# Optimization experiments

Measured on AMD Instinct MI355X. Metric: run time of the kernel, lower is better.

Reference implementation:

```python
import jax, jax.numpy as jnp
import numpy as np

B, T = 4, 96
IN_DIM, OUT_DIM, HID = 16, 16, 16
REL = 2 * IN_DIM  # until=True -> cat(interval max, interval min)
BIG = 1e9


def interval_pooling(a, reduction):
    # a: [b, t, t, d]; out[b,i,j] = reduce over a[b,k,l] for all i<=k<=l<=j
    t = a.shape[1]
    mask = jnp.triu(jnp.ones((t, t), dtype=bool))[None, :, :, None]
    if reduction == 'max':
        fill, cum = -BIG, jax.lax.cummax
    else:
        fill, cum = BIG, jax.lax.cummin
    x = jnp.where(mask, a, fill)
    x = cum(x, axis=1, reverse=True)  # over start k >= i
    x = cum(x, axis=2)                # over end   l <= j
    return jnp.where(mask, x, 0.0)


def dp_step(f, r, W, b):
    # linear_input[b,i,k,j] = cat(f[b,i,k], r[b,k,j]); MLPLogic = Linear+sigmoid;
    # transition_pooling_2d1d = max over k (dim 2). Split W so the wide cubic
    # concat is never materialized (same math as cat + matmul).
    df = f.shape[-1]
    Wf, Wr = W[:df], W[df:]
    ft = jnp.einsum('bikd,dh->bikh', f, Wf)[:, :, :, None, :]  # [b,i,k,1,h]
    rt = jnp.einsum('bkjd,dh->bkjh', r, Wr)[:, None, :, :, :]  # [b,1,k,j,h]
    g = jax.nn.sigmoid(ft + rt + b)  # [b, t+1, t+1, t+1, h] cubic intermediate
    return jnp.max(g, axis=2)        # pool over transition point k


def setup_inputs() -> dict:
    key = jax.random.key(0)
    ks = jax.random.split(key, 7)
    a = jax.random.normal(ks[0], (B, T, T, IN_DIM), jnp.float32)
    W0 = 0.1 * jax.random.normal(ks[1], (REL + REL, HID), jnp.float32)
    b0 = 0.1 * jax.random.normal(ks[2], (HID,), jnp.float32)
    W1 = 0.1 * jax.random.normal(ks[3], (HID + REL + REL, HID), jnp.float32)
    b1 = 0.1 * jax.random.normal(ks[4], (HID,), jnp.float32)
    W2 = 0.1 * jax.random.normal(ks[5], (HID + REL, OUT_DIM), jnp.float32)
    b2 = 0.1 * jax.random.normal(ks[6], (OUT_DIM,), jnp.float32)
    return {'a': a, 'W0': W0, 'b0': b0, 'W1': W1, 'b1': b1, 'W2': W2, 'b2': b2}


def reference(a, W0, b0, W1, b1, W2, b2):
    bsz, t = a.shape[0], a.shape[1]
    r = jnp.concatenate([interval_pooling(a, 'max'),
                         interval_pooling(a, 'min')], axis=-1)  # [b,t,t,2*in]
    f = jnp.zeros((bsz, t + 1, t + 1, r.shape[-1]), a.dtype)
    f = f.at[:, :-1, 1:].set(r)  # pad to boundary indexing [b,t+1,t+1,rel]
    r = f
    # step 0
    f = dp_step(f, r, W0, b0)
    f = jnp.concatenate([f, r], axis=-1)  # residual_input
    # step 1
    f = dp_step(f, r, W1, b1)
    f = jnp.concatenate([f, r], axis=-1)
    # final MLPLogic
    f = jax.nn.sigmoid(f @ W2 + b2)
    return f[:, :-1, 1:]
```

## Files before the change

kernel.cpp:

```cpp
#include <hip/hip_runtime.h>
#include <hip/hip_bf16.h>

#define RS   100
#define PLS  9700
#define NP   9409
#define LSTR 34

#define OFF_R   0
#define OFF_A   (OFF_R  + 4*32*PLS)
#define OFF_Bm  (OFF_A  + 4*16*PLS)
#define OFF_F1  (OFF_Bm + 4*16*PLS)
#define OFF_F2  (OFF_F1 + 4*16*PLS)

__device__ __forceinline__ float sigm(float x) { return 1.0f / (1.0f + __expf(-x)); }

__global__ __launch_bounds__(256) void pool_kernel(const float* __restrict__ a, float* __restrict__ R) {
    __shared__ float s[96][97];
    const int tid = threadIdx.x;
    const int b  = blockIdx.x >> 5;
    const int ch = blockIdx.x & 31;
    const int d  = ch & 15;
    const bool isMin = (ch >= 16);

    for (int idx = tid; idx < 96 * 96; idx += 256) {
        int i = idx / 96, j = idx - i * 96;
        float v = a[((size_t)(b * 96 + i) * 96 + j) * 16 + d];
        if (isMin) v = -v;
        s[i][j] = (j >= i) ? v : -1e30f;
    }
    __syncthreads();
    if (tid < 96) {
        int j = tid; float run = -1e30f;
#pragma unroll 4
        for (int i = 95; i >= 0; --i) { run = fmaxf(run, s[i][j]); s[i][j] = run; }
    }
    __syncthreads();
    if (tid < 96) {
        int i = tid; float run = -1e30f;
#pragma unroll 4
        for (int j = 0; j < 96; ++j) { run = fmaxf(run, s[i][j]); s[i][j] = run; }
    }
    __syncthreads();
    float* Rp = R + (size_t)blockIdx.x * PLS;
    for (int idx = tid; idx < 97 * 97; idx += 256) {
        int x = idx / 97, y = idx - x * 97;
        float v = 0.f;
        if (x <= 95 && y >= 1 && x <= y - 1) { v = s[x][y - 1]; if (isMin) v = -v; }
        Rp[x * RS + y] = v;
    }
}

__global__ __launch_bounds__(256) void proj0_kernel(const float* __restrict__ R, const float* __restrict__ W,
                                                    float* __restrict__ A, float* __restrict__ B) {
    const int by = blockIdx.y, b = by >> 3, hp = by & 7;
    const int h0 = hp * 2, h1 = h0 + 1;
    const int p = blockIdx.x * 256 + threadIdx.x;
    if (p >= NP) return;
    const int x = p / 97, y = p - x * 97;
    const int off = x * RS + y;
    const float* Rb = R + (size_t)b * 32 * PLS + off;
    float accA0 = 0.f, accA1 = 0.f, accB0 = 0.f, accB1 = 0.f;
#pragma unroll
    for (int d = 0; d < 32; ++d) {
        float rv = Rb[(size_t)d * PLS];
        accA0 += rv * W[d * 16 + h0];
        accA1 += rv * W[d * 16 + h1];
        accB0 += rv * W[(32 + d) * 16 + h0];
        accB1 += rv * W[(32 + d) * 16 + h1];
    }
    A[(size_t)(b * 16 + h0) * PLS + off] = accA0;
    A[(size_t)(b * 16 + h1) * PLS + off] = accA1;
    B[(size_t)(b * 16 + h0) * PLS + off] = accB0;
    B[(size_t)(b * 16 + h1) * PLS + off] = accB1;
}

__global__ __launch_bounds__(256) void proj1_kernel(const float* __restrict__ R, const float* __restrict__ F1,
                                                    const float* __restrict__ W,
                                                    float* __restrict__ A, float* __restrict__ B) {
    const int by = blockIdx.y, b = by >> 3, hp = by & 7;
    const int h0 = hp * 2, h1 = h0 + 1;
    const int p = blockIdx.x * 256 + threadIdx.x;
    if (p >= NP) return;
    const int x = p / 97, y = p - x * 97;
    const int off = x * RS + y;
    const float* Rb = R  + (size_t)b * 32 * PLS + off;
    const float* Fb = F1 + (size_t)b * 16 * PLS + off;
    float accA0 = 0.f, accA1 = 0.f, accB0 = 0.f, accB1 = 0.f;
#pragma unroll
    for (int c = 0; c < 16; ++c) {
        float fv = Fb[(size_t)c * PLS];
        accA0 += fv * W[c * 16 + h0];
        accA1 += fv * W[c * 16 + h1];
    }
#pragma unroll
    for (int d = 0; d < 32; ++d) {
        float rv = Rb[(size_t)d * PLS];
        accA0 += rv * W[(16 + d) * 16 + h0];
        accA1 += rv * W[(16 + d) * 16 + h1];
        accB0 += rv * W[(48 + d) * 16 + h0];
        accB1 += rv * W[(48 + d) * 16 + h1];
    }
    A[(size_t)(b * 16 + h0) * PLS + off] = accA0;
    A[(size_t)(b * 16 + h1) * PLS + off] = accA1;
    B[(size_t)(b * 16 + h0) * PLS + off] = accB0;
    B[(size_t)(b * 16 + h1) * PLS + off] = accB1;
}

__global__ __launch_bounds__(256) void maxplus_kernel(const float* __restrict__ A, const float* __restrict__ Bm,
                                                      const float* __restrict__ bias, float* __restrict__ F) {
    __shared__ alignas(16) float As[97 * LSTR];
    __shared__ alignas(16) float Bs[97 * LSTR];
    const int tid = threadIdx.x;
    const int bh = blockIdx.y;
    const int h  = bh & 15;
    const int i0 = (blockIdx.x & 3) * 32;
    const int j0 = (blockIdx.x >> 2) * 32;
    const float* Ab = A  + (size_t)bh * PLS;
    const float* Bb = Bm + (size_t)bh * PLS;

    for (int idx = tid; idx < 32 * 97; idx += 256) {
        int r = idx / 97, k = idx - r * 97;
        int ii = i0 + r;
        As[k * LSTR + r] = (ii < 97) ? Ab[ii * RS + k] : -1e30f;
    }
    for (int idx = tid; idx < 97 * 32; idx += 256) {
        int k = idx >> 5, c = idx & 31;
        int jj = j0 + c;
        Bs[k * LSTR + c] = (jj < 97) ? Bb[k * RS + jj] : -1e30f;
    }
    __syncthreads();

    const int ty = tid >> 4, tx = tid & 15;
    float a00 = -1e30f, a01 = -1e30f, a10 = -1e30f, a11 = -1e30f;

#pragma unroll 4
    for (int k = 0; k < 97; ++k) {
        const float2 a2 = *reinterpret_cast<const float2*>(&As[k * LSTR + ty * 2]);
        const float2 b2 = *reinterpret_cast<const float2*>(&Bs[k * LSTR + tx * 2]);
        a00 = fmaxf(a00, a2.x + b2.x);
        a01 = fmaxf(a01, a2.x + b2.y);
        a10 = fmaxf(a10, a2.y + b2.x);
        a11 = fmaxf(a11, a2.y + b2.y);
    }

    const float bb = bias[h];
    float* Fb = F + (size_t)bh * PLS;
    const int col0 = j0 + tx * 2;
    const int row0 = i0 + ty * 2;
    float v[2][2] = {{a00, a01}, {a10, a11}};
#pragma unroll
    for (int r = 0; r < 2; ++r) {
        const int row = row0 + r;
        if (row > 96) continue;
        if (col0 + 1 <= 96) {
            float2 o;
            o.x = sigm(v[r][0] + bb);
            o.y = sigm(v[r][1] + bb);
            *reinterpret_cast<float2*>(&Fb[row * RS + col0]) = o;
        } else if (col0 <= 96) {
            Fb[row * RS + col0] = sigm(v[r][0] + bb);
        }
    }
}

__global__ __launch_bounds__(256) void final_kernel(const float* __restrict__ R, const float* __restrict__ F2,
                                                    const float* __restrict__ W, const float* __restrict__ bias,
                                                    float* __restrict__ out) {
    const int p = blockIdx.x * 256 + threadIdx.x;
    if (p >= 4 * 96 * 96) return;
    const int oj = p % 96;
    const int t1 = p / 96;
    const int i  = t1 % 96;
    const int b  = t1 / 96;
    const int off = i * RS + (oj + 1);
    const float* Fb = F2 + (size_t)b * 16 * PLS + off;
    const float* Rb = R  + (size_t)b * 32 * PLS + off;
    float acc[16];
#pragma unroll
    for (int o = 0; o < 16; ++o) acc[o] = bias[o];
#pragma unroll
    for (int c = 0; c < 16; ++c) {
        const float fv = Fb[(size_t)c * PLS];
#pragma unroll
        for (int o = 0; o < 16; ++o) acc[o] += fv * W[c * 16 + o];
    }
#pragma unroll
    for (int d = 0; d < 32; ++d) {
        const float rv = Rb[(size_t)d * PLS];
#pragma unroll
        for (int o = 0; o < 16; ++o) acc[o] += rv * W[(16 + d) * 16 + o];
    }
    float4* dst = reinterpret_cast<float4*>(out + (size_t)p * 16);
#pragma unroll
    for (int q = 0; q < 4; ++q) {
        float4 v;
        v.x = sigm(acc[q * 4 + 0]);
        v.y = sigm(acc[q * 4 + 1]);
        v.z = sigm(acc[q * 4 + 2]);
        v.w = sigm(acc[q * 4 + 3]);
        dst[q] = v;
    }
}

extern "C" void kernel_launch(void* const* d_in, const int* in_sizes, int n_in,
                              void* d_out, int out_size, void* d_ws, size_t ws_size,
                              hipStream_t stream) {
    const float* a  = (const float*)d_in[0];
    const float* W0 = (const float*)d_in[1];
    const float* b0 = (const float*)d_in[2];
    const float* W1 = (const float*)d_in[3];
    const float* b1 = (const float*)d_in[4];
    const float* W2 = (const float*)d_in[5];
    const float* b2 = (const float*)d_in[6];
    float* ws = (float*)d_ws;
    float* out = (float*)d_out;

    hipLaunchKernelGGL(pool_kernel, dim3(128), dim3(256), 0, stream, a, ws + OFF_R);
    hipLaunchKernelGGL(proj0_kernel, dim3(37, 32), dim3(256), 0, stream,
                       ws + OFF_R, W0, ws + OFF_A, ws + OFF_Bm);
    hipLaunchKernelGGL(maxplus_kernel, dim3(16, 64), dim3(256), 0, stream,
                       ws + OFF_A, ws + OFF_Bm, b0, ws + OFF_F1);
    hipLaunchKernelGGL(proj1_kernel, dim3(37, 32), dim3(256), 0, stream,
                       ws + OFF_R, ws + OFF_F1, W1, ws + OFF_A, ws + OFF_Bm);
    hipLaunchKernelGGL(maxplus_kernel, dim3(16, 64), dim3(256), 0, stream,
                       ws + OFF_A, ws + OFF_Bm, b1, ws + OFF_F2);
    hipLaunchKernelGGL(final_kernel, dim3(144), dim3(256), 0, stream,
                       ws + OFF_R, ws + OFF_F2, W2, b2, out);
}
```

Measured before the change: 151.1 us.

## Precompute step-1 R projections early, widen maxplus tiles, split final kernel outputs

The R-dependent parts of both DP steps' projections are computed together in one kernel, so the second projection only adds the F1 contribution and re-reads far less of R. The max-plus kernel now gives each thread a 2x4 output tile with float4 B loads, which halves the block count and raises arithmetic per shared load. The final kernel spreads each output position over four threads, each producing four channels, to increase parallelism. In exchange the workspace holds two extra buffers and there is an extra read of the precomputed partial sums.

Measured after the change: 152.4 us. No clear change (+0.8%).

```diff
diff --git a/kernel.cpp b/kernel.cpp
--- a/kernel.cpp
+++ b/kernel.cpp
@@ -1,16 +1,18 @@
 #include <hip/hip_runtime.h>
-#include <hip/hip_bf16.h>
 
 #define RS   100
 #define PLS  9700
 #define NP   9409
-#define LSTR 34
+#define ASTR 34
+#define BSTR 68
 
 #define OFF_R   0
-#define OFF_A   (OFF_R  + 4*32*PLS)
-#define OFF_Bm  (OFF_A  + 4*16*PLS)
-#define OFF_F1  (OFF_Bm + 4*16*PLS)
-#define OFF_F2  (OFF_F1 + 4*16*PLS)
+#define OFF_A   (OFF_R   + 4*32*PLS)
+#define OFF_Bm  (OFF_A   + 4*16*PLS)
+#define OFF_F1  (OFF_Bm  + 4*16*PLS)
+#define OFF_F2  (OFF_F1  + 4*16*PLS)
+#define OFF_A1r (OFF_F2  + 4*16*PLS)
+#define OFF_B1  (OFF_A1r + 4*16*PLS)
 
 __device__ __forceinline__ float sigm(float x) { return 1.0f / (1.0f + __expf(-x)); }
 
@@ -50,8 +52,10 @@
     }
 }
 
-__global__ __launch_bounds__(256) void proj0_kernel(const float* __restrict__ R, const float* __restrict__ W,
-                                                    float* __restrict__ A, float* __restrict__ B) {
+__global__ __launch_bounds__(256) void projA_kernel(const float* __restrict__ R,
+                                                    const float* __restrict__ W0, const float* __restrict__ W1,
+                                                    float* __restrict__ A0, float* __restrict__ B0,
+                                                    float* __restrict__ A1r, float* __restrict__ B1) {
     const int by = blockIdx.y, b = by >> 3, hp = by & 7;
     const int h0 = hp * 2, h1 = h0 + 1;
     const int p = blockIdx.x * 256 + threadIdx.x;
@@ -59,106 +63,125 @@
     const int x = p / 97, y = p - x * 97;
     const int off = x * RS + y;
     const float* Rb = R + (size_t)b * 32 * PLS + off;
-    float accA0 = 0.f, accA1 = 0.f, accB0 = 0.f, accB1 = 0.f;
+    float aA00 = 0.f, aA01 = 0.f, aB00 = 0.f, aB01 = 0.f;
+    float aA10 = 0.f, aA11 = 0.f, aB10 = 0.f, aB11 = 0.f;
 #pragma unroll
     for (int d = 0; d < 32; ++d) {
-        float rv = Rb[(size_t)d * PLS];
-        accA0 += rv * W[d * 16 + h0];
-        accA1 += rv * W[d * 16 + h1];
-        accB0 += rv * W[(32 + d) * 16 + h0];
-        accB1 += rv * W[(32 + d) * 16 + h1];
-    }
-    A[(size_t)(b * 16 + h0) * PLS + off] = accA0;
-    A[(size_t)(b * 16 + h1) * PLS + off] = accA1;
-    B[(size_t)(b * 16 + h0) * PLS + off] = accB0;
-    B[(size_t)(b * 16 + h1) * PLS + off] = accB1;
-}
-
-__global__ __launch_bounds__(256) void proj1_kernel(const float* __restrict__ R, const float* __restrict__ F1,
-                                                    const float* __restrict__ W,
-                                                    float* __restrict__ A, float* __restrict__ B) {
+        const float rv = Rb[(size_t)d * PLS];
+        aA00 += rv * W0[d * 16 + h0];
+        aA01 += rv * W0[d * 16 + h1];
+        aB00 += rv * W0[(32 + d) * 16 + h0];
+        aB01 += rv * W0[(32 + d) * 16 + h1];
+        aA10 += rv * W1[(16 + d) * 16 + h0];
+        aA11 += rv * W1[(16 + d) * 16 + h1];
+        aB10 += rv * W1[(48 + d) * 16 + h0];
+        aB11 += rv * W1[(48 + d) * 16 + h1];
+    }
+    const size_t o0 = (size_t)(b * 16 + h0) * PLS + off;
+    const size_t o1 = (size_t)(b * 16 + h1) * PLS + off;
+    A0 [o0] = aA00;  A0 [o1] = aA01;
+    B0 [o0] = aB00;  B0 [o1] = aB01;
+    A1r[o0] = aA10;  A1r[o1] = aA11;
+    B1 [o0] = aB10;  B1 [o1] = aB11;
+}
+
+__global__ __launch_bounds__(256) void projF_kernel(const float* __restrict__ F1, const float* __restrict__ A1r,
+                                                    const float* __restrict__ W1, float* __restrict__ A) {
     const int by = blockIdx.y, b = by >> 3, hp = by & 7;
     const int h0 = hp * 2, h1 = h0 + 1;
     const int p = blockIdx.x * 256 + threadIdx.x;
     if (p >= NP) return;
     const int x = p / 97, y = p - x * 97;
     const int off = x * RS + y;
-    const float* Rb = R  + (size_t)b * 32 * PLS + off;
     const float* Fb = F1 + (size_t)b * 16 * PLS + off;
-    float accA0 = 0.f, accA1 = 0.f, accB0 = 0.f, accB1 = 0.f;
+    const size_t o0 = (size_t)(b * 16 + h0) * PLS + off;
+    const size_t o1 = (size_t)(b * 16 + h1) * PLS + off;
+    float a0 = A1r[o0], a1 = A1r[o1];
 #pragma unroll
     for (int c = 0; c < 16; ++c) {
-        float fv = Fb[(size_t)c * PLS];
-        accA0 += fv * W[c * 16 + h0];
-        accA1 += fv * W[c * 16 + h1];
-    }
-#pragma unroll
-    for (int d = 0; d < 32; ++d) {
-        float rv = Rb[(size_t)d * PLS];
-        accA0 += rv * W[(16 + d) * 16 + h0];
-        accA1 += rv * W[(16 + d) * 16 + h1];
-        accB0 += rv * W[(48 + d) * 16 + h0];
-        accB1 += rv * W[(48 + d) * 16 + h1];
-    }
-    A[(size_t)(b * 16 + h0) * PLS + off] = accA0;
-    A[(size_t)(b * 16 + h1) * PLS + off] = accA1;
-    B[(size_t)(b * 16 + h0) * PLS + off] = accB0;
-    B[(size_t)(b * 16 + h1) * PLS + off] = accB1;
+        const float fv = Fb[(size_t)c * PLS];
+        a0 += fv * W1[c * 16 + h0];
+        a1 += fv * W1[c * 16 + h1];
+    }
+    A[o0] = a0;
+    A[o1] = a1;
 }
 
 __global__ __launch_bounds__(256) void maxplus_kernel(const float* __restrict__ A, const float* __restrict__ Bm,
                                                       const float* __restrict__ bias, float* __restrict__ F) {
-    __shared__ alignas(16) float As[97 * LSTR];
-    __shared__ alignas(16) float Bs[97 * LSTR];
+    __shared__ alignas(16) float As[97 * ASTR];
+    __shared__ alignas(16) float Bs[97 * BSTR];
     const int tid = threadIdx.x;
     const int bh = blockIdx.y;
     const int h  = bh & 15;
     const int i0 = (blockIdx.x & 3) * 32;
-    const int j0 = (blockIdx.x >> 2) * 32;
+    const int j0 = (blockIdx.x >> 2) * 64;
     const float* Ab = A  + (size_t)bh * PLS;
     const float* Bb = Bm + (size_t)bh * PLS;
 
     for (int idx = tid; idx < 32 * 97; idx += 256) {
         int r = idx / 97, k = idx - r * 97;
         int ii = i0 + r;
-        As[k * LSTR + r] = (ii < 97) ? Ab[ii * RS + k] : -1e30f;
-    }
-    for (int idx = tid; idx < 97 * 32; idx += 256) {
-        int k = idx >> 5, c = idx & 31;
-        int jj = j0 + c;
-        Bs[k * LSTR + c] = (jj < 97) ? Bb[k * RS + jj] : -1e30f;
+        As[k * ASTR + r] = (ii <= 96) ? Ab[ii * RS + k] : -1e30f;
+    }
+    for (int idx = tid; idx < 97 * 16; idx += 256) {
+        int k = idx >> 4, q = idx & 15;
+        int jj = j0 + q * 4;
+        float4 v;
+        if (jj + 3 <= 96) {
+            v = *reinterpret_cast<const float4*>(&Bb[k * RS + jj]);
+        } else {
+            v.x = (jj     <= 96) ? Bb[k * RS + jj]     : -1e30f;
+            v.y = (jj + 1 <= 96) ? Bb[k * RS + jj + 1] : -1e30f;
+            v.z = (jj + 2 <= 96) ? Bb[k * RS + jj + 2] : -1e30f;
+            v.w = -1e30f;
+        }
+        *reinterpret_cast<float4*>(&Bs[k * BSTR + q * 4]) = v;
     }
     __syncthreads();
 
     const int ty = tid >> 4, tx = tid & 15;
-    float a00 = -1e30f, a01 = -1e30f, a10 = -1e30f, a11 = -1e30f;
+    float acc[2][4];
+#pragma unroll
+    for (int r = 0; r < 2; ++r)
+#pragma unroll
+        for (int c = 0; c < 4; ++c) acc[r][c] = -1e30f;
 
 #pragma unroll 4
     for (int k = 0; k < 97; ++k) {
-        const float2 a2 = *reinterpret_cast<const float2*>(&As[k * LSTR + ty * 2]);
-        const float2 b2 = *reinterpret_cast<const float2*>(&Bs[k * LSTR + tx * 2]);
-        a00 = fmaxf(a00, a2.x + b2.x);
-        a01 = fmaxf(a01, a2.x + b2.y);
-        a10 = fmaxf(a10, a2.y + b2.x);
-        a11 = fmaxf(a11, a2.y + b2.y);
+        const float2 a2 = *reinterpret_cast<const float2*>(&As[k * ASTR + ty * 2]);
+        const float4 b4 = *reinterpret_cast<const float4*>(&Bs[k * BSTR + tx * 4]);
+        acc[0][0] = fmaxf(acc[0][0], a2.x + b4.x);
+        acc[0][1] = fmaxf(acc[0][1], a2.x + b4.y);
+        acc[0][2] = fmaxf(acc[0][2], a2.x + b4.z);
+        acc[0][3] = fmaxf(acc[0][3], a2.x + b4.w);
+        acc[1][0] = fmaxf(acc[1][0], a2.y + b4.x);
+        acc[1][1] = fmaxf(acc[1][1], a2.y + b4.y);
+        acc[1][2] = fmaxf(acc[1][2], a2.y + b4.z);
+        acc[1][3] = fmaxf(acc[1][3], a2.y + b4.w);
     }
 
     const float bb = bias[h];
     float* Fb = F + (size_t)bh * PLS;
-    const int col0 = j0 + tx * 2;
     const int row0 = i0 + ty * 2;
-    float v[2][2] = {{a00, a01}, {a10, a11}};
+    const int col0 = j0 + tx * 4;
 #pragma unroll
     for (int r = 0; r < 2; ++r) {
         const int row = row0 + r;
         if (row > 96) continue;
-        if (col0 + 1 <= 96) {
-            float2 o;
-            o.x = sigm(v[r][0] + bb);
-            o.y = sigm(v[r][1] + bb);
-            *reinterpret_cast<float2*>(&Fb[row * RS + col0]) = o;
-        } else if (col0 <= 96) {
-            Fb[row * RS + col0] = sigm(v[r][0] + bb);
+        if (col0 + 3 <= 96) {
+            float4 o;
+            o.x = sigm(acc[r][0] + bb);
+            o.y = sigm(acc[r][1] + bb);
+            o.z = sigm(acc[r][2] + bb);
+            o.w = sigm(acc[r][3] + bb);
+            *reinterpret_cast<float4*>(&Fb[row * RS + col0]) = o;
+        } else {
+#pragma unroll
+            for (int c = 0; c < 4; ++c) {
+                const int col = col0 + c;
+                if (col <= 96) Fb[row * RS + col] = sigm(acc[r][c] + bb);
+            }
         }
     }
 }
@@ -166,8 +189,9 @@
 __global__ __launch_bounds__(256) void final_kernel(const float* __restrict__ R, const float* __restrict__ F2,
                                                     const float* __restrict__ W, const float* __restrict__ bias,
                                                     float* __restrict__ out) {
-    const int p = blockIdx.x * 256 + threadIdx.x;
-    if (p >= 4 * 96 * 96) return;
+    const int g = blockIdx.x * 256 + threadIdx.x;
+    const int p  = g >> 2;
+    const int oq = g & 3;
     const int oj = p % 96;
     const int t1 = p / 96;
     const int i  = t1 % 96;
@@ -175,31 +199,27 @@
     const int off = i * RS + (oj + 1);
     const float* Fb = F2 + (size_t)b * 16 * PLS + off;
     const float* Rb = R  + (size_t)b * 32 * PLS + off;
-    float acc[16];
-#pragma unroll
-    for (int o = 0; o < 16; ++o) acc[o] = bias[o];
+    float acc[4];
+#pragma unroll
+    for (int m = 0; m < 4; ++m) acc[m] = bias[oq * 4 + m];
 #pragma unroll
     for (int c = 0; c < 16; ++c) {
         const float fv = Fb[(size_t)c * PLS];
 #pragma unroll
-        for (int o = 0; o < 16; ++o) acc[o] += fv * W[c * 16 + o];
+        for (int m = 0; m < 4; ++m) acc[m] += fv * W[c * 16 + oq * 4 + m];
     }
 #pragma unroll
     for (int d = 0; d < 32; ++d) {
         const float rv = Rb[(size_t)d * PLS];
 #pragma unroll
-        for (int o = 0; o < 16; ++o) acc[o] += rv * W[(16 + d) * 16 + o];
-    }
-    float4* dst = reinterpret_cast<float4*>(out + (size_t)p * 16);
-#pragma unroll
-    for (int q = 0; q < 4; ++q) {
-        float4 v;
-        v.x = sigm(acc[q * 4 + 0]);
-        v.y = sigm(acc[q * 4 + 1]);
-        v.z = sigm(acc[q * 4 + 2]);
-        v.w = sigm(acc[q * 4 + 3]);
-        dst[q] = v;
-    }
+        for (int m = 0; m < 4; ++m) acc[m] += rv * W[(16 + d) * 16 + oq * 4 + m];
+    }
+    float4 v;
+    v.x = sigm(acc[0]);
+    v.y = sigm(acc[1]);
+    v.z = sigm(acc[2]);
+    v.w = sigm(acc[3]);
+    *reinterpret_cast<float4*>(out + (size_t)p * 16 + oq * 4) = v;
 }
 
 extern "C" void kernel_launch(void* const* d_in, const int* in_sizes, int n_in,
@@ -212,18 +232,18 @@
     const float* b1 = (const float*)d_in[4];
     const float* W2 = (const float*)d_in[5];
     const float* b2 = (const float*)d_in[6];
-    float* ws = (float*)d_ws;
+    float* ws  = (float*)d_ws;
     float* out = (float*)d_out;
 
     hipLaunchKernelGGL(pool_kernel, dim3(128), dim3(256), 0, stream, a, ws + OFF_R);
-    hipLaunchKernelGGL(proj0_kernel, dim3(37, 32), dim3(256), 0, stream,
-                       ws + OFF_R, W0, ws + OFF_A, ws + OFF_Bm);
-    hipLaunchKernelGGL(maxplus_kernel, dim3(16, 64), dim3(256), 0, stream,
+    hipLaunchKernelGGL(projA_kernel, dim3(37, 32), dim3(256), 0, stream,
+                       ws + OFF_R, W0, W1, ws + OFF_A, ws + OFF_Bm, ws + OFF_A1r, ws + OFF_B1);
+    hipLaunchKernelGGL(maxplus_kernel, dim3(8, 64), dim3(256), 0, stream,
                        ws + OFF_A, ws + OFF_Bm, b0, ws + OFF_F1);
-    hipLaunchKernelGGL(proj1_kernel, dim3(37, 32), dim3(256), 0, stream,
-                       ws + OFF_R, ws + OFF_F1, W1, ws + OFF_A, ws + OFF_Bm);
-    hipLaunchKernelGGL(maxplus_kernel, dim3(16, 64), dim3(256), 0, stream,
-                       ws + OFF_A, ws + OFF_Bm, b1, ws + OFF_F2);
-    hipLaunchKernelGGL(final_kernel, dim3(144), dim3(256), 0, stream,
+    hipLaunchKernelGGL(projF_kernel, dim3(37, 32), dim3(256), 0, stream,
+                       ws + OFF_F1, ws + OFF_A1r, W1, ws + OFF_A);
+    hipLaunchKernelGGL(maxplus_kernel, dim3(8, 64), dim3(256), 0, stream,
+                       ws + OFF_A, ws + OFF_B1, b1, ws + OFF_F2);
+    hipLaunchKernelGGL(final_kernel, dim3(576), dim3(256), 0, stream,
                        ws + OFF_R, ws + OFF_F2, W2, b2, out);
 }
```
